# Kernel optimization log

Measured on AMD Instinct MI355X. Metric: run time of the kernel, lower is better.

## Reference

```python
import jax, jax.numpy as jnp
import numpy as np

N = 50000          # nodes
E = 1_600_000      # edges (avg degree 32)
IN = 128           # in_channels
H = 2              # heads
C = 64             # out_channels per head


def setup_inputs() -> dict:
    key = jax.random.key(0)
    k = jax.random.split(key, 6)
    x = jax.random.normal(k[0], (N, IN), dtype=jnp.float32)
    edge_index = jax.random.randint(k[1], (2, E), 0, N, dtype=jnp.int32)
    W = jax.random.normal(k[2], (IN, H * C), dtype=jnp.float32) / np.sqrt(IN).astype(np.float32)
    att_src = jax.random.normal(k[3], (H, C), dtype=jnp.float32) * 0.1
    att_dst = jax.random.normal(k[4], (H, C), dtype=jnp.float32) * 0.1
    bias = jnp.zeros((C,), dtype=jnp.float32)
    return {"x": x, "W": W, "att_src": att_src, "att_dst": att_dst,
            "bias": bias, "edge_index": edge_index}


def reference(x, W, att_src, att_dst, bias, edge_index):
    Nn = x.shape[0]
    # linear projection per head: [N, H, C]
    h = (x @ W).reshape(Nn, H, C)
    # PyG GATConv default: add self loops
    loops = jnp.arange(Nn, dtype=edge_index.dtype)
    src = jnp.concatenate([edge_index[0], loops])  # [E+N]
    dst = jnp.concatenate([edge_index[1], loops])
    # per-node attention logits: a_src . h, a_dst . h -> [N, H]
    a_s = jnp.sum(h * att_src, axis=-1)
    a_d = jnp.sum(h * att_dst, axis=-1)
    # per-edge score, leaky relu (slope 0.2)
    e = jax.nn.leaky_relu(a_s[src] + a_d[dst], 0.2)  # [E+N, H]
    # softmax over incoming edges per destination node
    emax = jax.lax.stop_gradient(jax.ops.segment_max(e, dst, num_segments=Nn))
    e = jnp.exp(e - emax[dst])
    esum = jax.ops.segment_sum(e, dst, num_segments=Nn)
    alpha = e / (esum[dst] + 1e-16)                  # [E+N, H]
    # attention-weighted message passing: scatter-sum to destinations
    out = jax.ops.segment_sum(h[src] * alpha[:, :, None], dst, num_segments=Nn)  # [N, H, C]
    # concat=False -> mean over heads, then bias
    return out.mean(axis=1) + bias  # [N, C]
```

## Files before the change

### kernel.cpp

```cpp
#include <hip/hip_runtime.h>
#include <hip/hip_bf16.h>


#define NBLK 256
#define TH 512
#define BSH 7
#define BSZ 128
#define MAXBUCK 512
#define PLCAP 8192

typedef __attribute__((ext_vector_type(8))) short bf16x8;
typedef __attribute__((ext_vector_type(4))) float f32x4;

__device__ __forceinline__ ushort f2bf(float f) {
  __hip_bfloat16 b = __float2bfloat16(f);
  union { __hip_bfloat16 b; ushort u; } cv; cv.b = b; return cv.u;
}
__device__ __forceinline__ uint pk2(float a, float b) {
  return (uint)f2bf(a) | ((uint)f2bf(b) << 16);
}
__device__ __forceinline__ float leaky02(float v) {
  return fmaxf(v, 0.2f * v);
}

__global__ __launch_bounds__(128) void k_wa(const float* __restrict__ W,
                                            const float* __restrict__ as,
                                            const float* __restrict__ ad,
                                            ushort* __restrict__ wa) {
  const int k = threadIdx.x;
  float s0 = 0.f, s1 = 0.f, d0 = 0.f, d1 = 0.f;
  const float* wr = &W[k * 128];
  for (int c = 0; c < 64; ++c) {
    float w0 = wr[c], w1 = wr[64 + c];
    s0 = fmaf(w0, as[c], s0);
    s1 = fmaf(w1, as[64 + c], s1);
    d0 = fmaf(w0, ad[c], d0);
    d1 = fmaf(w1, ad[64 + c], d1);
  }
  wa[k * 4 + 0] = f2bf(s0);
  wa[k * 4 + 1] = f2bf(s1);
  wa[k * 4 + 2] = f2bf(d0);
  wa[k * 4 + 3] = f2bf(d1);
}

__global__ __launch_bounds__(256) void k_gemm(
    const float* __restrict__ x, const float* __restrict__ W,
    const ushort* __restrict__ wa, char* __restrict__ hq,
    float* __restrict__ scl, float* __restrict__ a_s,
    float* __restrict__ a_d, int Nn) {
  __shared__ ushort Al[64 * 128];
  __shared__ uint rmaxu[64];
  char* lb = (char*)Al;
  const int wave = threadIdx.x >> 6;
  const int lane = threadIdx.x & 63;
  const int row0 = blockIdx.x * 64;
  const int l15 = lane & 15;
  const int kb = (lane >> 4) * 8;

  if (threadIdx.x < 64) rmaxu[threadIdx.x] = 0u;

  {
    const int t = threadIdx.x;
    const int srow = t >> 2, q = t & 3;
    int gr = row0 + srow; gr = (gr < Nn) ? gr : (Nn - 1);
    const float4* xr = (const float4*)&x[(size_t)gr * 128 + q * 32];
#pragma unroll
    for (int i = 0; i < 4; ++i) {
      float4 v0 = xr[2 * i], v1 = xr[2 * i + 1];
      uint4 w;
      w.x = pk2(v0.x, v0.y); w.y = pk2(v0.z, v0.w);
      w.z = pk2(v1.x, v1.y); w.w = pk2(v1.z, v1.w);
      int byte = srow * 256 + ((q * 64 + i * 16) ^ ((srow & 7) << 4));
      *(uint4*)(lb + byte) = w;
    }
  }

  bf16x8 bfr[2][4];
#pragma unroll
  for (int c = 0; c < 2; ++c) {
#pragma unroll
    for (int ks = 0; ks < 4; ++ks) {
      const float* wp = &W[(ks * 32 + kb) * 128 + wave * 32 + c * 16 + l15];
      union { bf16x8 v; ushort u[8]; } t;
#pragma unroll
      for (int j = 0; j < 8; ++j) t.u[j] = f2bf(wp[j * 128]);
      bfr[c][ks] = t.v;
    }
  }
  bf16x8 wafr[4];
  if (wave == 3) {
#pragma unroll
    for (int ks = 0; ks < 4; ++ks) {
      union { bf16x8 v; ushort u[8]; } t;
#pragma unroll
      for (int j = 0; j < 8; ++j)
        t.u[j] = (l15 < 4) ? wa[(ks * 32 + kb + j) * 4 + l15] : (ushort)0;
      wafr[ks] = t.v;
    }
  }

  __syncthreads();

  f32x4 acc[4][2];
  f32x4 accwa[4];
#pragma unroll
  for (int r = 0; r < 4; ++r) {
    acc[r][0] = (f32x4){0.f, 0.f, 0.f, 0.f};
    acc[r][1] = (f32x4){0.f, 0.f, 0.f, 0.f};
    accwa[r] = (f32x4){0.f, 0.f, 0.f, 0.f};
  }
#pragma unroll
  for (int ks = 0; ks < 4; ++ks) {
    bf16x8 af[4];
#pragma unroll
    for (int r = 0; r < 4; ++r) {
      int row = r * 16 + l15;
      int byte = row * 256 + ((ks * 64 + (lane >> 4) * 16) ^ ((row & 7) << 4));
      uint4 v = *(const uint4*)(lb + byte);
      union { uint4 q; bf16x8 v; } cv; cv.q = v;
      af[r] = cv.v;
    }
#pragma unroll
    for (int r = 0; r < 4; ++r) {
      acc[r][0] = __builtin_amdgcn_mfma_f32_16x16x32_bf16(af[r], bfr[0][ks],
                                                          acc[r][0], 0, 0, 0);
      acc[r][1] = __builtin_amdgcn_mfma_f32_16x16x32_bf16(af[r], bfr[1][ks],
                                                          acc[r][1], 0, 0, 0);
    }
    if (wave == 3) {
#pragma unroll
      for (int r = 0; r < 4; ++r)
        accwa[r] = __builtin_amdgcn_mfma_f32_16x16x32_bf16(af[r], wafr[ks],
                                                           accwa[r], 0, 0, 0);
    }
  }

  const int rbase = (lane >> 4) * 4;
  float rm[4][4];
#pragma unroll
  for (int r = 0; r < 4; ++r)
#pragma unroll
    for (int i = 0; i < 4; ++i)
      rm[r][i] = fmaxf(fabsf(acc[r][0][i]), fabsf(acc[r][1][i]));
#pragma unroll
  for (int m = 1; m <= 8; m <<= 1) {
#pragma unroll
    for (int r = 0; r < 4; ++r)
#pragma unroll
      for (int i = 0; i < 4; ++i)
        rm[r][i] = fmaxf(rm[r][i], __shfl_xor(rm[r][i], m, 64));
  }
  __syncthreads();
  if (l15 == 0) {
#pragma unroll
    for (int r = 0; r < 4; ++r)
#pragma unroll
      for (int i = 0; i < 4; ++i)
        atomicMax(&rmaxu[r * 16 + rbase + i], __float_as_uint(rm[r][i]));
  }
  __syncthreads();

  char* Q = (char*)Al;
#pragma unroll
  for (int r = 0; r < 4; ++r) {
#pragma unroll
    for (int i = 0; i < 4; ++i) {
      const int lrow = r * 16 + rbase + i;
      const float inv = 127.f / fmaxf(__uint_as_float(rmaxu[lrow]), 1e-20f);
#pragma unroll
      for (int c = 0; c < 2; ++c) {
        const int col = wave * 32 + c * 16 + l15;
        int qv = __float2int_rn(acc[r][c][i] * inv);
        qv = (qv > 127) ? 127 : ((qv < -127) ? -127 : qv);
        Q[lrow * 128 + col] = (char)qv;
      }
    }
  }
  if (threadIdx.x < 64) {
    const int grow = row0 + threadIdx.x;
    if (grow < Nn)
      scl[grow] = __uint_as_float(rmaxu[threadIdx.x]) * (1.f / 127.f);
  }
  if (wave == 3) {
#pragma unroll
    for (int r = 0; r < 4; ++r) {
#pragma unroll
      for (int i = 0; i < 4; ++i) {
        int grow = row0 + r * 16 + rbase + i;
        if (grow < Nn) {
          float v = accwa[r][i];
          if (l15 < 2) a_s[grow * 2 + l15] = v;
          else if (l15 < 4) a_d[grow * 2 + (l15 - 2)] = v;
        }
      }
    }
  }
  __syncthreads();
#pragma unroll
  for (int k = 0; k < 2; ++k) {
    const int idx = threadIdx.x * 2 + k;
    const int row = idx >> 3;
    const int col = (idx & 7) * 16;
    uint4 v = *(const uint4*)(Q + row * 128 + col);
    if (row0 + row < Nn)
      *(uint4*)&hq[(size_t)(row0 + row) * 128 + col] = v;
  }
}

__global__ __launch_bounds__(TH) void k_bhist(const int* __restrict__ dst,
                                              int* __restrict__ bhist, int E,
                                              int nbuck, int chunk) {
  __shared__ int hl[MAXBUCK];
  for (int i = threadIdx.x; i < nbuck; i += TH) hl[i] = 0;
  __syncthreads();
  const int s = blockIdx.x * chunk;
  const int e = (s + chunk < E) ? s + chunk : E;
  for (int i = s + threadIdx.x; i < e; i += TH)
    atomicAdd(&hl[dst[i] >> BSH], 1);
  __syncthreads();
  for (int b = threadIdx.x; b < nbuck; b += TH)
    bhist[b * NBLK + blockIdx.x] = hl[b];
}

__global__ __launch_bounds__(NBLK) void k_bscan(const int* __restrict__ bhist,
                                                int* __restrict__ cursors,
                                                int* __restrict__ totals,
                                                int nbuck) {
  __shared__ int tmp[NBLK];
  const int b = blockIdx.x;
  const int t = threadIdx.x;
  const int v = bhist[b * NBLK + t];
  tmp[t] = v;
  __syncthreads();
  for (int d = 1; d < NBLK; d <<= 1) {
    int add = (t >= d) ? tmp[t - d] : 0;
    __syncthreads();
    tmp[t] += add;
    __syncthreads();
  }
  cursors[t * nbuck + b] = tmp[t] - v;
  if (t == NBLK - 1) totals[b] = tmp[t];
}

__global__ __launch_bounds__(MAXBUCK) void k_bbase(const int* __restrict__ totals,
                                                   int* __restrict__ bases,
                                                   int nbuck) {
  __shared__ int tmp[MAXBUCK];
  const int t = threadIdx.x;
  const int v = (t < nbuck) ? totals[t] : 0;
  tmp[t] = v;
  __syncthreads();
  for (int d = 1; d < MAXBUCK; d <<= 1) {
    int add = (t >= d) ? tmp[t - d] : 0;
    __syncthreads();
    tmp[t] += add;
    __syncthreads();
  }
  if (t < nbuck) bases[t] = tmp[t] - v;
  if (t == nbuck - 1) bases[nbuck] = tmp[t];
}

__global__ __launch_bounds__(TH) void k_binsert(
    const int* __restrict__ src, const int* __restrict__ dst,
    const int* __restrict__ cursors, const int* __restrict__ bases,
    int* __restrict__ pairs, int E, int nbuck, int chunk) {
  __shared__ int cur[MAXBUCK];
  for (int i = threadIdx.x; i < nbuck; i += TH)
    cur[i] = cursors[blockIdx.x * nbuck + i] + bases[i];
  __syncthreads();
  const int s = blockIdx.x * chunk;
  const int e = (s + chunk < E) ? s + chunk : E;
  for (int i = s + threadIdx.x; i < e; i += TH) {
    const int d = dst[i];
    const int b = d >> BSH;
    const int p = atomicAdd(&cur[b], 1);
    pairs[p] = ((d & (BSZ - 1)) << 16) | src[i];
  }
}

__global__ __launch_bounds__(256) void k_bucket(
    const int* __restrict__ pairs, const int* __restrict__ bases,
    int* __restrict__ off, int* __restrict__ cnt, int* __restrict__ csr,
    int Nn) {
  __shared__ int pl[PLCAP];
  __shared__ int cl[BSZ];
  __shared__ int tmp[BSZ];
  __shared__ int cu[BSZ];
  const int b = blockIdx.x;
  const int t = threadIdx.x;
  const int n0 = b << BSH;
  if (t < BSZ) cl[t] = 0;
  __syncthreads();
  const int s = bases[b], e = bases[b + 1];
  const int len = e - s;
  const bool fit = (len <= PLCAP);
  if (fit) {
    for (int i = t; i < len; i += 256) {
      int pv = pairs[s + i];
      pl[i] = pv;
      atomicAdd(&cl[pv >> 16], 1);
    }
  } else {
    for (int i = s + t; i < e; i += 256) atomicAdd(&cl[pairs[i] >> 16], 1);
  }
  __syncthreads();
  int v = 0;
  if (t < BSZ) { v = cl[t]; tmp[t] = v; }
  __syncthreads();
  for (int d = 1; d < BSZ; d <<= 1) {
    int add = (t < BSZ && t >= d) ? tmp[t - d] : 0;
    __syncthreads();
    if (t < BSZ) tmp[t] += add;
    __syncthreads();
  }
  if (t < BSZ) {
    const int excl = tmp[t] - v;
    cu[t] = s + excl;
    const int node = n0 + t;
    if (node < Nn) { off[node] = s + excl; cnt[node] = v; }
  }
  __syncthreads();
  if (fit) {
    for (int i = t; i < len; i += 256) {
      const int pv = pl[i];
      const int p = atomicAdd(&cu[pv >> 16], 1);
      csr[p] = pv & 0xffff;
    }
  } else {
    for (int i = s + t; i < e; i += 256) {
      const int pv = pairs[i];
      const int p = atomicAdd(&cu[pv >> 16], 1);
      csr[p] = pv & 0xffff;
    }
  }
}

__global__ __launch_bounds__(256) void k_aggr(
    const char* __restrict__ hq, const float* __restrict__ scl,
    const float* __restrict__ a_s, const float* __restrict__ a_d,
    const int* __restrict__ off, const int* __restrict__ cnt,
    const int* __restrict__ csr, const float* __restrict__ bias,
    float* __restrict__ out, int Nn) {
  __shared__ uint2 ewA[4][64];
  __shared__ uint2 ewB[4][64];
  const int wave = threadIdx.x >> 6;
  const int lane = threadIdx.x & 63;
  const int d = blockIdx.x * 4 + wave;
  if (d >= Nn) return;
  const int o = off[d];
  const int deg = cnt[d];
  const float2 ad2 = *(const float2*)&a_d[d * 2];
  const unsigned l2 = lane * 2u;
  const uint4* ebase = (lane < 32) ? (const uint4*)&ewA[wave][0]
                                   : (const uint4*)&ewB[wave][0];
  float acc0 = 0.f, acc1 = 0.f;
  float sw0 = 0.f, sw1 = 0.f;

  for (int c = 0; c < deg; c += 64) {
    int rem = deg - c; if (rem > 64) rem = 64;
    {
      unsigned voff = 0; float w0 = 0.f, w1 = 0.f, ws0 = 0.f, ws1 = 0.f;
      if (lane < rem) {
        int sl = csr[o + c + lane];
        float2 as2 = *(const float2*)&a_s[sl * 2];
        w0 = __expf(leaky02(as2.x + ad2.x));
        w1 = __expf(leaky02(as2.y + ad2.y));
        float s = scl[sl];
        voff = (unsigned)sl << 7;
        sw0 += w0; sw1 += w1;
        ws0 = w0 * s; ws1 = w1 * s;
      }
      ewA[wave][lane] = make_uint2(voff, __float_as_uint(ws0));
      ewB[wave][lane] = make_uint2(voff, __float_as_uint(ws1));
    }
    const int nq = (rem + 1) >> 1;
    int q = 0;
    for (; q + 4 <= nq; q += 4) {
      uint4 p0 = ebase[q + 0], p1 = ebase[q + 1];
      uint4 p2 = ebase[q + 2], p3 = ebase[q + 3];
      ushort a0 = *(const ushort*)(hq + (size_t)(p0.x + l2));
      ushort b0 = *(const ushort*)(hq + (size_t)(p0.z + l2));
      ushort a1 = *(const ushort*)(hq + (size_t)(p1.x + l2));
      ushort b1 = *(const ushort*)(hq + (size_t)(p1.z + l2));
      ushort a2 = *(const ushort*)(hq + (size_t)(p2.x + l2));
      ushort b2 = *(const ushort*)(hq + (size_t)(p2.z + l2));
      ushort a3 = *(const ushort*)(hq + (size_t)(p3.x + l2));
      ushort b3 = *(const ushort*)(hq + (size_t)(p3.z + l2));
      float wA0 = __uint_as_float(p0.y), wB0 = __uint_as_float(p0.w);
      float wA1 = __uint_as_float(p1.y), wB1 = __uint_as_float(p1.w);
      float wA2 = __uint_as_float(p2.y), wB2 = __uint_as_float(p2.w);
      float wA3 = __uint_as_float(p3.y), wB3 = __uint_as_float(p3.w);
      acc0 = fmaf(wA0, (float)(signed char)(a0 & 0xff), acc0);
      acc1 = fmaf(wA0, (float)(signed char)(a0 >> 8), acc1);
      acc0 = fmaf(wB0, (float)(signed char)(b0 & 0xff), acc0);
      acc1 = fmaf(wB0, (float)(signed char)(b0 >> 8), acc1);
      acc0 = fmaf(wA1, (float)(signed char)(a1 & 0xff), acc0);
      acc1 = fmaf(wA1, (float)(signed char)(a1 >> 8), acc1);
      acc0 = fmaf(wB1, (float)(signed char)(b1 & 0xff), acc0);
      acc1 = fmaf(wB1, (float)(signed char)(b1 >> 8), acc1);
      acc0 = fmaf(wA2, (float)(signed char)(a2 & 0xff), acc0);
      acc1 = fmaf(wA2, (float)(signed char)(a2 >> 8), acc1);
      acc0 = fmaf(wB2, (float)(signed char)(b2 & 0xff), acc0);
      acc1 = fmaf(wB2, (float)(signed char)(b2 >> 8), acc1);
      acc0 = fmaf(wA3, (float)(signed char)(a3 & 0xff), acc0);
      acc1 = fmaf(wA3, (float)(signed char)(a3 >> 8), acc1);
      acc0 = fmaf(wB3, (float)(signed char)(b3 & 0xff), acc0);
      acc1 = fmaf(wB3, (float)(signed char)(b3 >> 8), acc1);
    }
    for (; q < nq; ++q) {
      uint4 p = ebase[q];
      ushort va = *(const ushort*)(hq + (size_t)(p.x + l2));
      ushort vb = *(const ushort*)(hq + (size_t)(p.z + l2));
      float wA = __uint_as_float(p.y), wB = __uint_as_float(p.w);
      acc0 = fmaf(wA, (float)(signed char)(va & 0xff), acc0);
      acc1 = fmaf(wA, (float)(signed char)(va >> 8), acc1);
      acc0 = fmaf(wB, (float)(signed char)(vb & 0xff), acc0);
      acc1 = fmaf(wB, (float)(signed char)(vb >> 8), acc1);
    }
  }
#pragma unroll
  for (int msk = 1; msk <= 32; msk <<= 1) {
    sw0 += __shfl_xor(sw0, msk, 64);
    sw1 += __shfl_xor(sw1, msk, 64);
  }
  {
    float2 as2 = *(const float2*)&a_s[d * 2];
    float w0 = __expf(leaky02(as2.x + ad2.x));
    float w1 = __expf(leaky02(as2.y + ad2.y));
    sw0 += w0; sw1 += w1;
    float av = ((lane < 32) ? w0 : w1) * scl[d];
    ushort v = *(const ushort*)(hq + ((size_t)d << 7) + l2);
    acc0 = fmaf(av, (float)(signed char)(v & 0xff), acc0);
    acc1 = fmaf(av, (float)(signed char)(v >> 8), acc1);
  }
  const float invsel = 1.f / (((lane < 32) ? sw0 : sw1) + 1e-16f);
  acc0 *= invsel; acc1 *= invsel;
  float o0 = acc0 + __shfl_down(acc0, 32, 64);
  float o1 = acc1 + __shfl_down(acc1, 32, 64);
  if (lane < 32) {
    int c = lane * 2;
    float2 res = make_float2(0.5f * o0 + bias[c], 0.5f * o1 + bias[c + 1]);
    *(float2*)&out[(size_t)d * 64 + c] = res;
  }
}

extern "C" void kernel_launch(void* const* d_in, const int* in_sizes, int n_in,
                              void* d_out, int out_size, void* d_ws,
                              size_t ws_size, hipStream_t stream) {
  const float* x = (const float*)d_in[0];
  const float* W = (const float*)d_in[1];
  const float* att_s = (const float*)d_in[2];
  const float* att_d = (const float*)d_in[3];
  const float* bias = (const float*)d_in[4];
  const int* ei = (const int*)d_in[5];
  const int Nn = in_sizes[0] / 128;
  const int E = in_sizes[5] / 2;
  const int* src = ei;
  const int* dst = ei + E;
  float* out = (float*)d_out;

  const int nbuck = (Nn + BSZ - 1) >> BSH;
  const int chunk = (E + NBLK - 1) / NBLK;

  char* hq = (char*)d_ws;
  float* scl = (float*)(hq + (size_t)Nn * 128);
  float* a_s = scl + Nn;
  float* a_d = a_s + (size_t)Nn * 2;
  int* off = (int*)(a_d + (size_t)Nn * 2);
  int* cnt = off + Nn;
  int* bhist = cnt + Nn;
  int* cursors = bhist + (size_t)nbuck * NBLK;
  int* totals = cursors + (size_t)NBLK * nbuck;
  int* bases = totals + nbuck;
  ushort* wa = (ushort*)(bases + nbuck + 1);
  int* pairs = (int*)(wa + 512);
  int* csr = pairs + (size_t)E;

  hipLaunchKernelGGL(k_wa, dim3(1), dim3(128), 0, stream, W, att_s, att_d, wa);
  hipLaunchKernelGGL(k_gemm, dim3((Nn + 63) / 64), dim3(256), 0, stream, x, W,
                     wa, hq, scl, a_s, a_d, Nn);
  hipLaunchKernelGGL(k_bhist, dim3(NBLK), dim3(TH), 0, stream, dst, bhist, E,
                     nbuck, chunk);
  hipLaunchKernelGGL(k_bscan, dim3(nbuck), dim3(NBLK), 0, stream, bhist,
                     cursors, totals, nbuck);
  hipLaunchKernelGGL(k_bbase, dim3(1), dim3(MAXBUCK), 0, stream, totals, bases,
                     nbuck);
  hipLaunchKernelGGL(k_binsert, dim3(NBLK), dim3(TH), 0, stream, src, dst,
                     cursors, bases, pairs, E, nbuck, chunk);
  hipLaunchKernelGGL(k_bucket, dim3(nbuck), dim3(256), 0, stream, pairs, bases,
                     off, cnt, csr, Nn);
  hipLaunchKernelGGL(k_aggr, dim3((Nn + 3) / 4), dim3(256), 0, stream, hq, scl,
                     a_s, a_d, off, cnt, csr, bias, out, Nn);
}
```

Baseline: 111.3 us.

## Fuse weight-attention, GEMM and histogram kernels; pack per-node scalars; deepen gather unroll

Merges k_wa, k_gemm and k_bhist into one launch. The first NBLK blocks build the bucket histogram and the remaining blocks compute the attention-weight vector in shared memory and then run the GEMM. The base-offset scan is folded into k_binsert, which cuts launches from eight to five. Per-node a_s and scale are packed into one float4, so aggregation does a single 16-byte load per neighbor. The gather loop is unrolled to 8 pairs to put more loads in flight. The cost is that every GEMM block recomputes the W·att product, the scan is redone in each k_binsert block, and register pressure rises in k_aggr.

Measured after the change: 134.3 us. 20.7% more time.

```diff
diff --git a/kernel.cpp b/kernel.cpp
--- a/kernel.cpp
+++ b/kernel.cpp
@@ -23,41 +23,52 @@
   return fmaxf(v, 0.2f * v);
 }
 
-__global__ __launch_bounds__(128) void k_wa(const float* __restrict__ W,
-                                            const float* __restrict__ as,
-                                            const float* __restrict__ ad,
-                                            ushort* __restrict__ wa) {
-  const int k = threadIdx.x;
-  float s0 = 0.f, s1 = 0.f, d0 = 0.f, d1 = 0.f;
-  const float* wr = &W[k * 128];
-  for (int c = 0; c < 64; ++c) {
-    float w0 = wr[c], w1 = wr[64 + c];
-    s0 = fmaf(w0, as[c], s0);
-    s1 = fmaf(w1, as[64 + c], s1);
-    d0 = fmaf(w0, ad[c], d0);
-    d1 = fmaf(w1, ad[64 + c], d1);
-  }
-  wa[k * 4 + 0] = f2bf(s0);
-  wa[k * 4 + 1] = f2bf(s1);
-  wa[k * 4 + 2] = f2bf(d0);
-  wa[k * 4 + 3] = f2bf(d1);
-}
-
-__global__ __launch_bounds__(256) void k_gemm(
+__global__ __launch_bounds__(256) void k_mega(
     const float* __restrict__ x, const float* __restrict__ W,
-    const ushort* __restrict__ wa, char* __restrict__ hq,
-    float* __restrict__ scl, float* __restrict__ a_s,
-    float* __restrict__ a_d, int Nn) {
+    const float* __restrict__ att_s, const float* __restrict__ att_d,
+    char* __restrict__ hq, float4* __restrict__ asc, float* __restrict__ a_d,
+    int Nn, const int* __restrict__ dst, int* __restrict__ bhist, int E,
+    int nbuck, int chunkE) {
   __shared__ ushort Al[64 * 128];
   __shared__ uint rmaxu[64];
+  __shared__ ushort wal[512];
+
+  if ((int)blockIdx.x < NBLK) {
+    int* hl = (int*)Al;
+    const int bb = blockIdx.x;
+    for (int i = threadIdx.x; i < nbuck; i += 256) hl[i] = 0;
+    __syncthreads();
+    const int s = bb * chunkE;
+    const int e = (s + chunkE < E) ? s + chunkE : E;
+    for (int i = s + threadIdx.x; i < e; i += 256)
+      atomicAdd(&hl[dst[i] >> BSH], 1);
+    __syncthreads();
+    for (int b = threadIdx.x; b < nbuck; b += 256)
+      bhist[b * NBLK + bb] = hl[b];
+    return;
+  }
   char* lb = (char*)Al;
   const int wave = threadIdx.x >> 6;
   const int lane = threadIdx.x & 63;
-  const int row0 = blockIdx.x * 64;
+  const int row0 = ((int)blockIdx.x - NBLK) * 64;
   const int l15 = lane & 15;
   const int kb = (lane >> 4) * 8;
 
   if (threadIdx.x < 64) rmaxu[threadIdx.x] = 0u;
+
+  {
+    const int k = threadIdx.x >> 1;
+    const int pair = threadIdx.x & 1;
+    const float* av = pair ? att_d : att_s;
+    const float* wr = &W[k * 128];
+    float e0 = 0.f, e1 = 0.f;
+    for (int c = 0; c < 64; ++c) {
+      e0 = fmaf(wr[c], av[c], e0);
+      e1 = fmaf(wr[64 + c], av[64 + c], e1);
+    }
+    wal[k * 4 + pair * 2 + 0] = f2bf(e0);
+    wal[k * 4 + pair * 2 + 1] = f2bf(e1);
+  }
 
   {
     const int t = threadIdx.x;
@@ -87,6 +98,9 @@
       bfr[c][ks] = t.v;
     }
   }
+
+  __syncthreads();
+
   bf16x8 wafr[4];
   if (wave == 3) {
 #pragma unroll
@@ -94,12 +108,10 @@
       union { bf16x8 v; ushort u[8]; } t;
 #pragma unroll
       for (int j = 0; j < 8; ++j)
-        t.u[j] = (l15 < 4) ? wa[(ks * 32 + kb + j) * 4 + l15] : (ushort)0;
+        t.u[j] = (l15 < 4) ? wal[(ks * 32 + kb + j) * 4 + l15] : (ushort)0;
       wafr[ks] = t.v;
     }
   }
-
-  __syncthreads();
 
   f32x4 acc[4][2];
   f32x4 accwa[4];
@@ -176,21 +188,21 @@
       }
     }
   }
-  if (threadIdx.x < 64) {
-    const int grow = row0 + threadIdx.x;
-    if (grow < Nn)
-      scl[grow] = __uint_as_float(rmaxu[threadIdx.x]) * (1.f / 127.f);
-  }
   if (wave == 3) {
+    float* ascf = (float*)asc;
 #pragma unroll
     for (int r = 0; r < 4; ++r) {
 #pragma unroll
       for (int i = 0; i < 4; ++i) {
-        int grow = row0 + r * 16 + rbase + i;
+        const int lrow = r * 16 + rbase + i;
+        const int grow = row0 + lrow;
         if (grow < Nn) {
           float v = accwa[r][i];
-          if (l15 < 2) a_s[grow * 2 + l15] = v;
+          if (l15 < 2) ascf[(size_t)grow * 4 + l15] = v;
           else if (l15 < 4) a_d[grow * 2 + (l15 - 2)] = v;
+          else if (l15 == 4)
+            ascf[(size_t)grow * 4 + 2] =
+                __uint_as_float(rmaxu[lrow]) * (1.f / 127.f);
         }
       }
     }
@@ -205,21 +217,6 @@
     if (row0 + row < Nn)
       *(uint4*)&hq[(size_t)(row0 + row) * 128 + col] = v;
   }
-}
-
-__global__ __launch_bounds__(TH) void k_bhist(const int* __restrict__ dst,
-                                              int* __restrict__ bhist, int E,
-                                              int nbuck, int chunk) {
-  __shared__ int hl[MAXBUCK];
-  for (int i = threadIdx.x; i < nbuck; i += TH) hl[i] = 0;
-  __syncthreads();
-  const int s = blockIdx.x * chunk;
-  const int e = (s + chunk < E) ? s + chunk : E;
-  for (int i = s + threadIdx.x; i < e; i += TH)
-    atomicAdd(&hl[dst[i] >> BSH], 1);
-  __syncthreads();
-  for (int b = threadIdx.x; b < nbuck; b += TH)
-    bhist[b * NBLK + blockIdx.x] = hl[b];
 }
 
 __global__ __launch_bounds__(NBLK) void k_bscan(const int* __restrict__ bhist,
@@ -242,35 +239,33 @@
   if (t == NBLK - 1) totals[b] = tmp[t];
 }
 
-__global__ __launch_bounds__(MAXBUCK) void k_bbase(const int* __restrict__ totals,
-                                                   int* __restrict__ bases,
-                                                   int nbuck) {
-  __shared__ int tmp[MAXBUCK];
+__global__ __launch_bounds__(TH) void k_binsert(
+    const int* __restrict__ src, const int* __restrict__ dst,
+    const int* __restrict__ cursors, const int* __restrict__ totals,
+    int* __restrict__ bases, int* __restrict__ pairs, int E, int nbuck,
+    int chunk) {
+  __shared__ int bb[MAXBUCK];
+  __shared__ int cur[MAXBUCK];
   const int t = threadIdx.x;
   const int v = (t < nbuck) ? totals[t] : 0;
-  tmp[t] = v;
+  bb[t] = v;
   __syncthreads();
   for (int d = 1; d < MAXBUCK; d <<= 1) {
-    int add = (t >= d) ? tmp[t - d] : 0;
-    __syncthreads();
-    tmp[t] += add;
-    __syncthreads();
-  }
-  if (t < nbuck) bases[t] = tmp[t] - v;
-  if (t == nbuck - 1) bases[nbuck] = tmp[t];
-}
-
-__global__ __launch_bounds__(TH) void k_binsert(
-    const int* __restrict__ src, const int* __restrict__ dst,
-    const int* __restrict__ cursors, const int* __restrict__ bases,
-    int* __restrict__ pairs, int E, int nbuck, int chunk) {
-  __shared__ int cur[MAXBUCK];
-  for (int i = threadIdx.x; i < nbuck; i += TH)
-    cur[i] = cursors[blockIdx.x * nbuck + i] + bases[i];
+    int add = (t >= d) ? bb[t - d] : 0;
+    __syncthreads();
+    bb[t] += add;
+    __syncthreads();
+  }
+  const int base_t = bb[t] - v;
+  if (t < nbuck) cur[t] = cursors[blockIdx.x * nbuck + t] + base_t;
+  if (blockIdx.x == 0) {
+    if (t < nbuck) bases[t] = base_t;
+    if (t == nbuck - 1) bases[nbuck] = bb[t];
+  }
   __syncthreads();
   const int s = blockIdx.x * chunk;
   const int e = (s + chunk < E) ? s + chunk : E;
-  for (int i = s + threadIdx.x; i < e; i += TH) {
+  for (int i = s + t; i < e; i += TH) {
     const int d = dst[i];
     const int b = d >> BSH;
     const int p = atomicAdd(&cur[b], 1);
@@ -336,11 +331,10 @@
 }
 
 __global__ __launch_bounds__(256) void k_aggr(
-    const char* __restrict__ hq, const float* __restrict__ scl,
-    const float* __restrict__ a_s, const float* __restrict__ a_d,
-    const int* __restrict__ off, const int* __restrict__ cnt,
-    const int* __restrict__ csr, const float* __restrict__ bias,
-    float* __restrict__ out, int Nn) {
+    const char* __restrict__ hq, const float4* __restrict__ asc,
+    const float* __restrict__ a_d, const int* __restrict__ off,
+    const int* __restrict__ cnt, const int* __restrict__ csr,
+    const float* __restrict__ bias, float* __restrict__ out, int Nn) {
   __shared__ uint2 ewA[4][64];
   __shared__ uint2 ewB[4][64];
   const int wave = threadIdx.x >> 6;
@@ -362,34 +356,46 @@
       unsigned voff = 0; float w0 = 0.f, w1 = 0.f, ws0 = 0.f, ws1 = 0.f;
       if (lane < rem) {
         int sl = csr[o + c + lane];
-        float2 as2 = *(const float2*)&a_s[sl * 2];
-        w0 = __expf(leaky02(as2.x + ad2.x));
-        w1 = __expf(leaky02(as2.y + ad2.y));
-        float s = scl[sl];
+        float4 a4 = asc[sl];
+        w0 = __expf(leaky02(a4.x + ad2.x));
+        w1 = __expf(leaky02(a4.y + ad2.y));
         voff = (unsigned)sl << 7;
         sw0 += w0; sw1 += w1;
-        ws0 = w0 * s; ws1 = w1 * s;
+        ws0 = w0 * a4.z; ws1 = w1 * a4.z;
       }
       ewA[wave][lane] = make_uint2(voff, __float_as_uint(ws0));
       ewB[wave][lane] = make_uint2(voff, __float_as_uint(ws1));
     }
     const int nq = (rem + 1) >> 1;
     int q = 0;
-    for (; q + 4 <= nq; q += 4) {
+    for (; q + 8 <= nq; q += 8) {
+      uint4 p[8];
+#pragma unroll
+      for (int u = 0; u < 8; ++u) p[u] = ebase[q + u];
+      ushort va[8], vb[8];
+#pragma unroll
+      for (int u = 0; u < 8; ++u) {
+        va[u] = *(const ushort*)(hq + (size_t)(p[u].x + l2));
+        vb[u] = *(const ushort*)(hq + (size_t)(p[u].z + l2));
+      }
+#pragma unroll
+      for (int u = 0; u < 8; ++u) {
+        const float wA = __uint_as_float(p[u].y);
+        const float wB = __uint_as_float(p[u].w);
+        acc0 = fmaf(wA, (float)(signed char)(va[u] & 0xff), acc0);
+        acc1 = fmaf(wA, (float)(signed char)(va[u] >> 8), acc1);
+        acc0 = fmaf(wB, (float)(signed char)(vb[u] & 0xff), acc0);
+        acc1 = fmaf(wB, (float)(signed char)(vb[u] >> 8), acc1);
+      }
+    }
+    for (; q + 2 <= nq; q += 2) {
       uint4 p0 = ebase[q + 0], p1 = ebase[q + 1];
-      uint4 p2 = ebase[q + 2], p3 = ebase[q + 3];
       ushort a0 = *(const ushort*)(hq + (size_t)(p0.x + l2));
       ushort b0 = *(const ushort*)(hq + (size_t)(p0.z + l2));
       ushort a1 = *(const ushort*)(hq + (size_t)(p1.x + l2));
       ushort b1 = *(const ushort*)(hq + (size_t)(p1.z + l2));
-      ushort a2 = *(const ushort*)(hq + (size_t)(p2.x + l2));
-      ushort b2 = *(const ushort*)(hq + (size_t)(p2.z + l2));
-      ushort a3 = *(const ushort*)(hq + (size_t)(p3.x + l2));
-      ushort b3 = *(const ushort*)(hq + (size_t)(p3.z + l2));
       float wA0 = __uint_as_float(p0.y), wB0 = __uint_as_float(p0.w);
       float wA1 = __uint_as_float(p1.y), wB1 = __uint_as_float(p1.w);
-      float wA2 = __uint_as_float(p2.y), wB2 = __uint_as_float(p2.w);
-      float wA3 = __uint_as_float(p3.y), wB3 = __uint_as_float(p3.w);
       acc0 = fmaf(wA0, (float)(signed char)(a0 & 0xff), acc0);
       acc1 = fmaf(wA0, (float)(signed char)(a0 >> 8), acc1);
       acc0 = fmaf(wB0, (float)(signed char)(b0 & 0xff), acc0);
@@ -398,14 +404,6 @@
       acc1 = fmaf(wA1, (float)(signed char)(a1 >> 8), acc1);
       acc0 = fmaf(wB1, (float)(signed char)(b1 & 0xff), acc0);
       acc1 = fmaf(wB1, (float)(signed char)(b1 >> 8), acc1);
-      acc0 = fmaf(wA2, (float)(signed char)(a2 & 0xff), acc0);
-      acc1 = fmaf(wA2, (float)(signed char)(a2 >> 8), acc1);
-      acc0 = fmaf(wB2, (float)(signed char)(b2 & 0xff), acc0);
-      acc1 = fmaf(wB2, (float)(signed char)(b2 >> 8), acc1);
-      acc0 = fmaf(wA3, (float)(signed char)(a3 & 0xff), acc0);
-      acc1 = fmaf(wA3, (float)(signed char)(a3 >> 8), acc1);
-      acc0 = fmaf(wB3, (float)(signed char)(b3 & 0xff), acc0);
-      acc1 = fmaf(wB3, (float)(signed char)(b3 >> 8), acc1);
     }
     for (; q < nq; ++q) {
       uint4 p = ebase[q];
@@ -424,11 +422,11 @@
     sw1 += __shfl_xor(sw1, msk, 64);
   }
   {
-    float2 as2 = *(const float2*)&a_s[d * 2];
-    float w0 = __expf(leaky02(as2.x + ad2.x));
-    float w1 = __expf(leaky02(as2.y + ad2.y));
+    float4 a4 = asc[d];
+    float w0 = __expf(leaky02(a4.x + ad2.x));
+    float w1 = __expf(leaky02(a4.y + ad2.y));
     sw0 += w0; sw1 += w1;
-    float av = ((lane < 32) ? w0 : w1) * scl[d];
+    float av = ((lane < 32) ? w0 : w1) * a4.z;
     ushort v = *(const ushort*)(hq + ((size_t)d << 7) + l2);
     acc0 = fmaf(av, (float)(signed char)(v & 0xff), acc0);
     acc1 = fmaf(av, (float)(signed char)(v >> 8), acc1);
@@ -461,34 +459,29 @@
 
   const int nbuck = (Nn + BSZ - 1) >> BSH;
   const int chunk = (E + NBLK - 1) / NBLK;
+  const int ngemm = (Nn + 63) / 64;
 
   char* hq = (char*)d_ws;
-  float* scl = (float*)(hq + (size_t)Nn * 128);
-  float* a_s = scl + Nn;
-  float* a_d = a_s + (size_t)Nn * 2;
+  float4* asc = (float4*)(hq + (size_t)Nn * 128);
+  float* a_d = (float*)(asc + Nn);
   int* off = (int*)(a_d + (size_t)Nn * 2);
   int* cnt = off + Nn;
   int* bhist = cnt + Nn;
   int* cursors = bhist + (size_t)nbuck * NBLK;
   int* totals = cursors + (size_t)NBLK * nbuck;
   int* bases = totals + nbuck;
-  ushort* wa = (ushort*)(bases + nbuck + 1);
-  int* pairs = (int*)(wa + 512);
+  int* pairs = bases + nbuck + 1;
   int* csr = pairs + (size_t)E;
 
-  hipLaunchKernelGGL(k_wa, dim3(1), dim3(128), 0, stream, W, att_s, att_d, wa);
-  hipLaunchKernelGGL(k_gemm, dim3((Nn + 63) / 64), dim3(256), 0, stream, x, W,
-                     wa, hq, scl, a_s, a_d, Nn);
-  hipLaunchKernelGGL(k_bhist, dim3(NBLK), dim3(TH), 0, stream, dst, bhist, E,
-                     nbuck, chunk);
+  hipLaunchKernelGGL(k_mega, dim3(NBLK + ngemm), dim3(256), 0, stream, x, W,
+                     att_s, att_d, hq, asc, a_d, Nn, dst, bhist, E, nbuck,
+                     chunk);
   hipLaunchKernelGGL(k_bscan, dim3(nbuck), dim3(NBLK), 0, stream, bhist,
                      cursors, totals, nbuck);
-  hipLaunchKernelGGL(k_bbase, dim3(1), dim3(MAXBUCK), 0, stream, totals, bases,
-                     nbuck);
   hipLaunchKernelGGL(k_binsert, dim3(NBLK), dim3(TH), 0, stream, src, dst,
-                     cursors, bases, pairs, E, nbuck, chunk);
+                     cursors, totals, bases, pairs, E, nbuck, chunk);
   hipLaunchKernelGGL(k_bucket, dim3(nbuck), dim3(256), 0, stream, pairs, bases,
                      off, cnt, csr, Nn);
-  hipLaunchKernelGGL(k_aggr, dim3((Nn + 3) / 4), dim3(256), 0, stream, hq, scl,
-                     a_s, a_d, off, cnt, csr, bias, out, Nn);
-}
+  hipLaunchKernelGGL(k_aggr, dim3((Nn + 3) / 4), dim3(256), 0, stream, hq, asc,
+                     a_d, off, cnt, csr, bias, out, Nn);
+}
```
